# Performance work log

Hardware: AMD Instinct MI355X
Metric: run time of the kernel (lower is better)

Reference implementation:

```python
import jax, jax.numpy as jnp
import numpy as np

B, N, D, H = 2, 2048, 128, 128  # batch, n_nodes, node_dim, hidden_dim
HQ = H // 4
EPS_DIST = 1e-8
EPS_LN = 1e-5


def setup_inputs() -> dict:
    key = jax.random.key(0)
    ks = jax.random.split(key, 12)
    s = 0.02
    return {
        "h": jax.random.normal(ks[0], (B, N, D), jnp.float32),
        "coords": jax.random.uniform(ks[1], (B, N, 2), jnp.float32),
        "Wq": jax.random.normal(ks[2], (D, H), jnp.float32) * s,
        "bq": jnp.zeros((H,), jnp.float32),
        "Wk": jax.random.normal(ks[3], (D, H), jnp.float32) * s,
        "bk": jnp.zeros((H,), jnp.float32),
        "Wv": jax.random.normal(ks[4], (D, H), jnp.float32) * s,
        "bv": jnp.zeros((H,), jnp.float32),
        "Wd1": jax.random.normal(ks[5], (1, HQ), jnp.float32) * s,
        "bd1": jnp.zeros((HQ,), jnp.float32),
        "Wd2": jax.random.normal(ks[6], (HQ, 1), jnp.float32) * s,
        "bd2": jnp.zeros((1,), jnp.float32),
        "Wo": jax.random.normal(ks[7], (H, D), jnp.float32) * s,
        "bo": jnp.zeros((D,), jnp.float32),
        "gamma": jnp.ones((D,), jnp.float32),
        "beta": jnp.zeros((D,), jnp.float32),
    }


def reference(h, coords, Wq, bq, Wk, bk, Wv, bv, Wd1, bd1, Wd2, bd2, Wo, bo, gamma, beta):
    q = h @ Wq + bq                      # (B, N, H)
    k = h @ Wk + bk
    v = h @ Wv + bv
    scores = jnp.einsum('bnh,bmh->bnm', q, k) / jnp.sqrt(jnp.float32(H))  # (B,N,N)
    # pairwise Euclidean distances
    diff = coords[:, :, None, :] - coords[:, None, :, :]                  # (B,N,N,2)
    dist = jnp.sqrt(jnp.sum(diff * diff, axis=-1, keepdims=True) + EPS_DIST)  # (B,N,N,1)
    hmid = jax.nn.silu(dist @ Wd1 + bd1)                                  # (B,N,N,HQ)
    dist_bias = (hmid @ Wd2 + bd2)[..., 0]                                # (B,N,N)
    attn = jax.nn.softmax(scores + dist_bias, axis=-1)
    out = jnp.einsum('bnm,bmh->bnh', attn, v)                             # (B,N,H)
    out = jax.nn.silu(out @ Wo + bo)                                      # (B,N,D)
    res = h + out
    mu = jnp.mean(res, axis=-1, keepdims=True)
    var = jnp.mean((res - mu) ** 2, axis=-1, keepdims=True)
    return (res - mu) / jnp.sqrt(var + EPS_LN) * gamma + beta
```

## Files before the change

### kernel.cpp

```cpp
#include <hip/hip_runtime.h>
#include <hip/hip_bf16.h>

#define B_ 2
#define N_ 2048
#define D_ 128
#define H_ 128
#define HQ_ 32
#define ROWS_ (B_*N_)
#define KS_ 16
#define KPP_ (N_/KS_)
#define DMAX_ 1.4143f
#define SCALE_ 0.08838834764831845f

typedef __bf16 bf16x8 __attribute__((ext_vector_type(8)));
typedef float  f32x4  __attribute__((ext_vector_type(4)));
typedef unsigned short ushort8 __attribute__((ext_vector_type(8)));

#define Q_OFF    0
#define K_OFF    (ROWS_*H_*2)
#define V_OFF    (2*ROWS_*H_*2)
#define L_OFF    (3*ROWS_*H_*2)
#define OP_OFF   (L_OFF + ROWS_*KS_*4)

__global__ __launch_bounds__(384) void qkv_kernel(
    const float* __restrict__ h,
    const float* __restrict__ Wq, const float* __restrict__ bq,
    const float* __restrict__ Wk, const float* __restrict__ bk,
    const float* __restrict__ Wv, const float* __restrict__ bv,
    __bf16* __restrict__ qb, __bf16* __restrict__ kb, __bf16* __restrict__ vb)
{
    __shared__ __align__(16) float hs[8][128];
    const int t = threadIdx.x;
    const int row0 = blockIdx.x * 8;
    for (int idx = t; idx < 1024; idx += 384) hs[idx >> 7][idx & 127] = h[row0 * 128 + idx];
    __syncthreads();

    const int which = t >> 7;
    const int c = t & 127;
    const float* W    = which == 0 ? Wq : (which == 1 ? Wk : Wv);
    const float* bias = which == 0 ? bq : (which == 1 ? bk : bv);
    __bf16* outp      = which == 0 ? qb : (which == 1 ? kb : vb);
    const float scale = which == 0 ? SCALE_ : 1.f;

    float acc[8];
    #pragma unroll
    for (int r = 0; r < 8; ++r) acc[r] = 0.f;

    #pragma unroll 8
    for (int d = 0; d < 128; ++d) {
        float w = W[d * 128 + c];
        #pragma unroll
        for (int r = 0; r < 8; ++r) acc[r] = fmaf(hs[r][d], w, acc[r]);
    }
    const float bvv = bias[c];
    #pragma unroll
    for (int r = 0; r < 8; ++r)
        outp[(size_t)(row0 + r) * 128 + c] = (__bf16)((acc[r] + bvv) * scale);
}

__global__ __launch_bounds__(256, 4) void attn_kernel(
    const __bf16* __restrict__ qb, const __bf16* __restrict__ kb, const __bf16* __restrict__ vb,
    const float* __restrict__ coords,
    const float* __restrict__ Wd1, const float* __restrict__ bd1,
    const float* __restrict__ Wd2, const float* __restrict__ bd2,
    __bf16* __restrict__ Opb, float* __restrict__ Larr)
{
    __shared__ __align__(16) unsigned int Vsu[2][128][20];
    __shared__ __align__(16) __bf16 Pl[4][16][40];

    const int t    = threadIdx.x;
    const int wid  = t >> 6;
    const int lane = t & 63;
    const int l16  = lane & 15;
    const int g    = lane >> 4;
    const int qbase = blockIdx.x * 64 + wid * 16;
    const int p     = blockIdx.y;
    const int b     = qbase >> 11;

    float c0, c1, c2, c3, c4;
    {
        const int j = lane & 31;
        const float w1 = Wd1[j], b1 = bd1[j];
        const float w2h = Wd2[j] * 0.5f;
        float gv[5];
        #pragma unroll
        for (int i = 0; i < 5; ++i) {
            float d = (DMAX_ * 0.25f) * (float)i;
            float x = fmaf(d, w1, b1);
            gv[i] = (x / (1.f + __expf(-x))) * w2h;
        }
        #pragma unroll
        for (int i = 0; i < 5; ++i)
            #pragma unroll
            for (int off = 1; off < 64; off <<= 1) gv[i] += __shfl_xor(gv[i], off);
        const float bd2v = bd2[0];
        float g0 = gv[0] + bd2v, g1 = gv[1] + bd2v, g2 = gv[2] + bd2v,
              g3 = gv[3] + bd2v, g4 = gv[4] + bd2v;
        c0 = g0;
        c1 = -2.0833333333f*g0 + 4.f*g1 - 3.f*g2 + 1.3333333333f*g3 - 0.25f*g4;
        c2 =  1.4583333333f*g0 - 4.3333333333f*g1 + 4.75f*g2 - 2.3333333333f*g3 + 0.4583333333f*g4;
        c3 = -0.4166666667f*g0 + 1.5f*g1 - 2.f*g2 + 1.1666666667f*g3 - 0.25f*g4;
        c4 =  0.0416666667f*g0 - 0.1666666667f*g1 + 0.25f*g2 - 0.1666666667f*g3 + 0.0416666667f*g4;
    }

    bf16x8 qf[4];
    const __bf16* qrow = qb + (size_t)(qbase + l16) * H_;
    #pragma unroll
    for (int kk = 0; kk < 4; ++kk) qf[kk] = *(const bf16x8*)(qrow + kk * 32 + g * 8);

    float cx[4], cy[4];
    #pragma unroll
    for (int i = 0; i < 4; ++i) {
        int qr = qbase + g * 4 + i;
        cx[i] = coords[qr * 2]; cy[i] = coords[qr * 2 + 1];
    }

    float l_i[4] = {0.f, 0.f, 0.f, 0.f};
    f32x4 O[8];
    #pragma unroll
    for (int c = 0; c < 8; ++c) O[c] = (f32x4){0.f, 0.f, 0.f, 0.f};

    const int kp = t & 15, co = t >> 4;
    const int kgbase = (b << 11) + p * KPP_;
    const int NT = KPP_ / 32;

    {
        const __bf16* sp = vb + (size_t)(kgbase + 2 * kp) * H_ + co * 8;
        bf16x8 va = *(const bf16x8*)sp;
        bf16x8 vb2 = *(const bf16x8*)(sp + H_);
        ushort8 ua = __builtin_bit_cast(ushort8, va);
        ushort8 ub = __builtin_bit_cast(ushort8, vb2);
        #pragma unroll
        for (int j = 0; j < 8; ++j)
            Vsu[0][co * 8 + j][kp] = (unsigned)ua[j] | ((unsigned)ub[j] << 16);
    }

    for (int kt = 0; kt < NT; ++kt) {
        __syncthreads();

        bf16x8 nva, nvb;
        if (kt + 1 < NT) {
            const __bf16* sp = vb + (size_t)(kgbase + (kt + 1) * 32 + 2 * kp) * H_ + co * 8;
            nva = *(const bf16x8*)sp;
            nvb = *(const bf16x8*)(sp + H_);
        }

        const int kg = kgbase + kt * 32;
        #pragma unroll
        for (int mt = 0; mt < 2; ++mt) {
            f32x4 acc = (f32x4){0.f, 0.f, 0.f, 0.f};
            const __bf16* krow = kb + (size_t)(kg + mt * 16 + l16) * H_;
            #pragma unroll
            for (int kk = 0; kk < 4; ++kk) {
                bf16x8 kf = *(const bf16x8*)(krow + kk * 32 + g * 8);
                acc = __builtin_amdgcn_mfma_f32_16x16x32_bf16(qf[kk], kf, acc, 0, 0, 0);
            }
            float2 kc = *(const float2*)&coords[(kg + mt * 16 + l16) * 2];
            #pragma unroll
            for (int i = 0; i < 4; ++i) {
                float dx = cx[i] - kc.x, dy = cy[i] - kc.y;
                float dist = sqrtf(fmaf(dx, dx, fmaf(dy, dy, 1e-8f)));
                float s4 = dist * (4.0f / DMAX_);
                float bias = fmaf(fmaf(fmaf(fmaf(c4, s4, c3), s4, c2), s4, c1), s4, c0);
                float sc = fminf(acc[i] + bias, 60.f);
                float pe = __expf(sc);
                l_i[i] += pe;
                Pl[wid][g * 4 + i][mt * 16 + l16] = (__bf16)pe;
            }
        }

        if (kt + 1 < NT) {
            ushort8 ua = __builtin_bit_cast(ushort8, nva);
            ushort8 ub = __builtin_bit_cast(ushort8, nvb);
            #pragma unroll
            for (int j = 0; j < 8; ++j)
                Vsu[(kt + 1) & 1][co * 8 + j][kp] = (unsigned)ua[j] | ((unsigned)ub[j] << 16);
        }

        bf16x8 pf = *(const bf16x8*)&Pl[wid][l16][g * 8];
        #pragma unroll
        for (int c = 0; c < 8; ++c) {
            bf16x8 vf = *(const bf16x8*)&Vsu[kt & 1][c * 16 + l16][g * 4];
            O[c] = __builtin_amdgcn_mfma_f32_16x16x32_bf16(pf, vf, O[c], 0, 0, 0);
        }
    }

    #pragma unroll
    for (int c = 0; c < 8; ++c)
        #pragma unroll
        for (int i = 0; i < 4; ++i)
            Opb[((size_t)p * ROWS_ + qbase + g * 4 + i) * H_ + c * 16 + l16] = (__bf16)O[c][i];

    #pragma unroll
    for (int i = 0; i < 4; ++i) {
        float lv = l_i[i];
        lv += __shfl_xor(lv, 1); lv += __shfl_xor(lv, 2);
        lv += __shfl_xor(lv, 4); lv += __shfl_xor(lv, 8);
        if (l16 == 0) Larr[(qbase + g * 4 + i) * KS_ + p] = lv;
    }
}

__global__ __launch_bounds__(128) void final_kernel(
    const __bf16* __restrict__ Opb, const float* __restrict__ Larr,
    const float* __restrict__ h, const float* __restrict__ Wo, const float* __restrict__ bo,
    const float* __restrict__ gamma, const float* __restrict__ beta, float* __restrict__ out)
{
    __shared__ __align__(16) float as_[4][128];
    __shared__ float redS[2][4], redQ[2][4];
    const int t = threadIdx.x;
    const int row0 = blockIdx.x * 4;

    #pragma unroll
    for (int r = 0; r < 4; ++r) {
        int row = row0 + r;
        float acc = 0.f, lsum = 0.f;
        #pragma unroll
        for (int p = 0; p < KS_; ++p) {
            acc  += (float)Opb[((size_t)p * ROWS_ + row) * H_ + t];
            lsum += Larr[row * KS_ + p];
        }
        as_[r][t] = acc / lsum;
    }
    __syncthreads();

    float acc4[4] = {0.f, 0.f, 0.f, 0.f};
    #pragma unroll 4
    for (int d4 = 0; d4 < 32; ++d4) {
        float w0 = Wo[(d4 * 4 + 0) * 128 + t];
        float w1 = Wo[(d4 * 4 + 1) * 128 + t];
        float w2 = Wo[(d4 * 4 + 2) * 128 + t];
        float w3 = Wo[(d4 * 4 + 3) * 128 + t];
        #pragma unroll
        for (int r = 0; r < 4; ++r) {
            f32x4 a_ = *(const f32x4*)&as_[r][d4 * 4];
            acc4[r] = fmaf(a_[0], w0, acc4[r]);
            acc4[r] = fmaf(a_[1], w1, acc4[r]);
            acc4[r] = fmaf(a_[2], w2, acc4[r]);
            acc4[r] = fmaf(a_[3], w3, acc4[r]);
        }
    }

    const float bov = bo[t], gv = gamma[t], bvv = beta[t];
    const int wh = t >> 6;
    float res[4];
    #pragma unroll
    for (int r = 0; r < 4; ++r) {
        float x = acc4[r] + bov;
        float sl = x / (1.f + __expf(-x));
        res[r] = h[(size_t)(row0 + r) * 128 + t] + sl;
    }

    #pragma unroll
    for (int r = 0; r < 4; ++r) {
        float s1 = res[r], s2 = res[r] * res[r];
        #pragma unroll
        for (int off = 32; off >= 1; off >>= 1) {
            s1 += __shfl_xor(s1, off);
            s2 += __shfl_xor(s2, off);
        }
        if ((t & 63) == 0) { redS[wh][r] = s1; redQ[wh][r] = s2; }
    }
    __syncthreads();
    #pragma unroll
    for (int r = 0; r < 4; ++r) {
        float sum = redS[0][r] + redS[1][r];
        float sq  = redQ[0][r] + redQ[1][r];
        float mu  = sum * (1.f / 128.f);
        float var = sq * (1.f / 128.f) - mu * mu;
        out[(size_t)(row0 + r) * 128 + t] = (res[r] - mu) * rsqrtf(var + 1e-5f) * gv + bvv;
    }
}

extern "C" void kernel_launch(void* const* d_in, const int* in_sizes, int n_in,
                              void* d_out, int out_size, void* d_ws, size_t ws_size,
                              hipStream_t stream)
{
    const float* h      = (const float*)d_in[0];
    const float* coords = (const float*)d_in[1];
    const float* Wq = (const float*)d_in[2];  const float* bq = (const float*)d_in[3];
    const float* Wk = (const float*)d_in[4];  const float* bk = (const float*)d_in[5];
    const float* Wv = (const float*)d_in[6];  const float* bv = (const float*)d_in[7];
    const float* Wd1 = (const float*)d_in[8]; const float* bd1 = (const float*)d_in[9];
    const float* Wd2 = (const float*)d_in[10];const float* bd2 = (const float*)d_in[11];
    const float* Wo = (const float*)d_in[12]; const float* bo = (const float*)d_in[13];
    const float* gamma = (const float*)d_in[14]; const float* beta = (const float*)d_in[15];

    char* ws = (char*)d_ws;
    __bf16* qb = (__bf16*)(ws + Q_OFF);
    __bf16* kb = (__bf16*)(ws + K_OFF);
    __bf16* vb = (__bf16*)(ws + V_OFF);
    float* Larr  = (float*)(ws + L_OFF);
    __bf16* Opb  = (__bf16*)(ws + OP_OFF);

    qkv_kernel<<<ROWS_ / 8, 384, 0, stream>>>(h, Wq, bq, Wk, bk, Wv, bv, qb, kb, vb);
    attn_kernel<<<dim3(ROWS_ / 64, KS_), 256, 0, stream>>>(qb, kb, vb, coords,
                                                           Wd1, bd1, Wd2, bd2, Opb, Larr);
    final_kernel<<<ROWS_ / 4, 128, 0, stream>>>(Opb, Larr, h, Wo, bo, gamma, beta, (float*)d_out);
}
```

Baseline: 59.12 us.

## Compute QKV projection with bf16 MFMA after converting h and transposing weights

Replaces the scalar fp32 FMA QKV projection kernel with two kernels. A prep kernel converts h to bf16 and transposes Wq/Wk/Wv into bf16 column-major tiles in workspace. A second kernel then computes the projection with 16x16x32 bf16 MFMA instructions. This moves the projection GEMM onto matrix cores, but adds an extra launch and a workspace round trip, and rounds h and the weights to bf16 before the multiply instead of after it.

```diff
diff --git a/kernel.cpp b/kernel.cpp
--- a/kernel.cpp
+++ b/kernel.cpp
@@ -12,6 +12,7 @@
 #define DMAX_ 1.4143f
 #define SCALE_ 0.08838834764831845f
 
+typedef __bf16 bf16x4 __attribute__((ext_vector_type(4)));
 typedef __bf16 bf16x8 __attribute__((ext_vector_type(8)));
 typedef float  f32x4  __attribute__((ext_vector_type(4)));
 typedef unsigned short ushort8 __attribute__((ext_vector_type(8)));
@@ -21,41 +22,87 @@
 #define V_OFF    (2*ROWS_*H_*2)
 #define L_OFF    (3*ROWS_*H_*2)
 #define OP_OFF   (L_OFF + ROWS_*KS_*4)
-
-__global__ __launch_bounds__(384) void qkv_kernel(
+#define HB_OFF   (OP_OFF + (size_t)ROWS_*KS_*H_*2)
+#define WT_OFF   (HB_OFF + ROWS_*D_*2)
+
+__global__ __launch_bounds__(256) void prep_kernel(
     const float* __restrict__ h,
-    const float* __restrict__ Wq, const float* __restrict__ bq,
-    const float* __restrict__ Wk, const float* __restrict__ bk,
-    const float* __restrict__ Wv, const float* __restrict__ bv,
+    const float* __restrict__ Wq, const float* __restrict__ Wk, const float* __restrict__ Wv,
+    __bf16* __restrict__ hb, __bf16* __restrict__ Wt)
+{
+    const int bid = blockIdx.x, t = threadIdx.x;
+    if (bid < 256) {
+        const float4* src = (const float4*)(h + (size_t)bid * 2048);
+        __bf16* dst = hb + (size_t)bid * 2048;
+        #pragma unroll
+        for (int i = 0; i < 2; ++i) {
+            float4 v = src[t + i * 256];
+            bf16x4 pk = { (__bf16)v.x, (__bf16)v.y, (__bf16)v.z, (__bf16)v.w };
+            *(bf16x4*)(dst + (t + i * 256) * 4) = pk;
+        }
+    } else {
+        __shared__ float tile[128][17];
+        const int id = bid - 256;
+        const int m = id >> 3, ch = id & 7;
+        const float* W = m == 0 ? Wq : (m == 1 ? Wk : Wv);
+        const int c0 = ch * 16;
+        #pragma unroll
+        for (int i = 0; i < 8; ++i) {
+            int idx = t + i * 256;
+            int k = idx >> 4, cc = idx & 15;
+            tile[k][cc] = W[k * 128 + c0 + cc];
+        }
+        __syncthreads();
+        __bf16* dst = Wt + m * 16384;
+        #pragma unroll
+        for (int i = 0; i < 8; ++i) {
+            int idx = t + i * 256;
+            int cc = idx >> 7, k = idx & 127;
+            dst[(c0 + cc) * 128 + k] = (__bf16)tile[k][cc];
+        }
+    }
+}
+
+__global__ __launch_bounds__(256) void qkv_mfma(
+    const __bf16* __restrict__ hb, const __bf16* __restrict__ Wt,
+    const float* __restrict__ bq, const float* __restrict__ bk, const float* __restrict__ bv,
     __bf16* __restrict__ qb, __bf16* __restrict__ kb, __bf16* __restrict__ vb)
 {
-    __shared__ __align__(16) float hs[8][128];
-    const int t = threadIdx.x;
-    const int row0 = blockIdx.x * 8;
-    for (int idx = t; idx < 1024; idx += 384) hs[idx >> 7][idx & 127] = h[row0 * 128 + idx];
-    __syncthreads();
-
-    const int which = t >> 7;
-    const int c = t & 127;
-    const float* W    = which == 0 ? Wq : (which == 1 ? Wk : Wv);
+    const int t = threadIdx.x, wid = t >> 6, lane = t & 63;
+    const int l16 = lane & 15, g = lane >> 4;
+    const int row0 = blockIdx.x * 64 + wid * 16;
+    const int co   = blockIdx.y * 32;
+    const int which = co >> 7, c0 = co & 127;
+    const __bf16* Wm = Wt + which * 16384;
+    __bf16* outp      = which == 0 ? qb : (which == 1 ? kb : vb);
     const float* bias = which == 0 ? bq : (which == 1 ? bk : bv);
-    __bf16* outp      = which == 0 ? qb : (which == 1 ? kb : vb);
     const float scale = which == 0 ? SCALE_ : 1.f;
 
-    float acc[8];
-    #pragma unroll
-    for (int r = 0; r < 8; ++r) acc[r] = 0.f;
-
-    #pragma unroll 8
-    for (int d = 0; d < 128; ++d) {
-        float w = W[d * 128 + c];
-        #pragma unroll
-        for (int r = 0; r < 8; ++r) acc[r] = fmaf(hs[r][d], w, acc[r]);
-    }
-    const float bvv = bias[c];
-    #pragma unroll
-    for (int r = 0; r < 8; ++r)
-        outp[(size_t)(row0 + r) * 128 + c] = (__bf16)((acc[r] + bvv) * scale);
+    bf16x8 af[4];
+    const __bf16* arow = hb + (size_t)(row0 + l16) * 128;
+    #pragma unroll
+    for (int kk = 0; kk < 4; ++kk) af[kk] = *(const bf16x8*)(arow + kk * 32 + g * 8);
+
+    f32x4 acc0 = {0.f,0.f,0.f,0.f}, acc1 = {0.f,0.f,0.f,0.f};
+    const __bf16* b0 = Wm + (size_t)(c0 + l16) * 128;
+    const __bf16* b1 = Wm + (size_t)(c0 + 16 + l16) * 128;
+    #pragma unroll
+    for (int kk = 0; kk < 4; ++kk) {
+        bf16x8 f0 = *(const bf16x8*)(b0 + kk * 32 + g * 8);
+        acc0 = __builtin_amdgcn_mfma_f32_16x16x32_bf16(af[kk], f0, acc0, 0, 0, 0);
+    }
+    #pragma unroll
+    for (int kk = 0; kk < 4; ++kk) {
+        bf16x8 f1 = *(const bf16x8*)(b1 + kk * 32 + g * 8);
+        acc1 = __builtin_amdgcn_mfma_f32_16x16x32_bf16(af[kk], f1, acc1, 0, 0, 0);
+    }
+    const float bv0 = bias[c0 + l16], bv1 = bias[c0 + 16 + l16];
+    #pragma unroll
+    for (int i = 0; i < 4; ++i) {
+        size_t r = (size_t)(row0 + g * 4 + i) * 128;
+        outp[r + c0 + l16]      = (__bf16)((acc0[i] + bv0) * scale);
+        outp[r + c0 + 16 + l16] = (__bf16)((acc1[i] + bv1) * scale);
+    }
 }
 
 __global__ __launch_bounds__(256, 4) void attn_kernel(
@@ -291,8 +338,11 @@
     __bf16* vb = (__bf16*)(ws + V_OFF);
     float* Larr  = (float*)(ws + L_OFF);
     __bf16* Opb  = (__bf16*)(ws + OP_OFF);
-
-    qkv_kernel<<<ROWS_ / 8, 384, 0, stream>>>(h, Wq, bq, Wk, bk, Wv, bv, qb, kb, vb);
+    __bf16* hb   = (__bf16*)(ws + HB_OFF);
+    __bf16* Wt   = (__bf16*)(ws + WT_OFF);
+
+    prep_kernel<<<280, 256, 0, stream>>>(h, Wq, Wk, Wv, hb, Wt);
+    qkv_mfma<<<dim3(ROWS_ / 64, 12), 256, 0, stream>>>(hb, Wt, bq, bk, bv, qb, kb, vb);
     attn_kernel<<<dim3(ROWS_ / 64, KS_), 256, 0, stream>>>(qb, kb, vb, coords,
                                                            Wd1, bd1, Wd2, bd2, Opb, Larr);
     final_kernel<<<ROWS_ / 4, 128, 0, stream>>>(Opb, Larr, h, Wo, bo, gamma, beta, (float*)d_out);
```

New measurement: 56.37 us. 1.05x faster.
